# Performance work log

Measured on AMD Instinct MI355X. Metric: run time of the kernel, lower is better.

The kernel has to match this reference:

```python
import jax, jax.numpy as jnp
import numpy as np

N, F, E, K = 2048, 32, 16, 32
SPARSITY = 0.05


def setup_inputs() -> dict:
    key = jax.random.key(0)
    ks = jax.random.split(key, 10)
    adj = (jax.random.uniform(ks[0], (N, N)) < SPARSITY).astype(jnp.float32)
    nodes_features = jax.random.normal(ks[1], (N, F), dtype=jnp.float32)
    edges_features = jax.random.normal(ks[2], (N, N, E), dtype=jnp.float32)
    s = 0.05
    W_ne = jax.random.normal(ks[3], (F + E, F), dtype=jnp.float32) * s
    b_ne = jnp.zeros((F,), dtype=jnp.float32)
    W_n = jax.random.normal(ks[4], (F, F), dtype=jnp.float32) * s
    b_n = jnp.zeros((F,), dtype=jnp.float32)
    W_net = jax.random.normal(ks[5], (F, K), dtype=jnp.float32) * s
    b_net = jnp.zeros((K,), dtype=jnp.float32)
    eps = jnp.zeros((1,), dtype=jnp.float32)
    return {"adj": adj, "nodes_features": nodes_features, "edges_features": edges_features,
            "W_ne": W_ne, "b_ne": b_ne, "W_n": W_n, "b_n": b_n,
            "W_net": W_net, "b_net": b_net, "eps": eps}


def reference(adj, nodes_features, edges_features, W_ne, b_ne, W_n, b_n, W_net, b_net, eps):
    # node_edge_net(cat([broadcast(nodes), edges])) == split matmul: avoids
    # materializing the [N,N,F+E] concat; the [N,N,F] output is still formed.
    Fdim = nodes_features.shape[-1]
    node_part = nodes_features @ W_ne[:Fdim]            # [N,F] -> broadcast over dim 0
    edge_part = jnp.einsum('ije,ef->ijf', edges_features, W_ne[Fdim:])  # [N,N,F]
    ne = jax.nn.relu(node_part[None, :, :] + edge_part + b_ne)          # [N,N,F]
    msg = jnp.einsum('ij,ijf->if', adj, ne)             # masked sum over neighbors j
    node_term = jax.nn.relu(nodes_features @ W_n + b_n)  # node_net
    out = (1.0 + eps) * node_term + msg
    out = jax.nn.relu(out @ W_net + b_net)               # self.net (FCLayer)
    return (adj, out, edges_features)
```

## Files before the change

### kernel.cpp

```cpp
#include <hip/hip_runtime.h>
#include <stdint.h>

#define NN 2048
#define FF 32
#define EE 16
#define KK 32
#define NCOPY 2048
#define TOTALB (2 * NN)

__global__ __launch_bounds__(256) void gin_fused_kernel(
    const float* __restrict__ adj,
    const float* __restrict__ nodes,
    const float* __restrict__ edges,
    const float* __restrict__ W_ne,
    const float* __restrict__ b_ne,
    const float* __restrict__ W_n,
    const float* __restrict__ b_n,
    const float* __restrict__ W_net,
    const float* __restrict__ b_net,
    const float* __restrict__ epsp,
    float* __restrict__ out_adj,
    float* __restrict__ out_y,
    float* __restrict__ out_edges)
{
    const int b   = blockIdx.x;
    const int tid = threadIdx.x;

    if (b & 1) {
        const int cb = b >> 1;
        const float4* __restrict__ src = (const float4*)edges;
        float4*       __restrict__ dst = (float4*)out_edges;
        const int per  = (NN * NN * EE / 4) / NCOPY;
        const int base = cb * per;
        #pragma unroll 8
        for (int t = tid; t < per; t += 256) dst[base + t] = src[base + t];
        return;
    }

    const int i = b >> 1;
    const int f = tid & 31;
    const int g = tid >> 5;

    __shared__ float swe[EE][FF];
    __shared__ float swn[FF][FF];
    __shared__ unsigned short sidx[NN];
    __shared__ float sval[NN];
    __shared__ float smsg[FF];
    __shared__ float sh[FF];
    __shared__ int scnt;

    for (int t = tid; t < EE * FF; t += 256) swe[t / FF][t % FF] = W_ne[FF * FF + t];
    for (int t = tid; t < FF * FF; t += 256) swn[t / FF][t % FF] = W_ne[t];
    if (tid == 0) scnt = 0;
    if (tid < FF) smsg[tid] = 0.0f;
    __syncthreads();

    const size_t arow = (size_t)i * NN;

    {
        const float4* src = (const float4*)(adj + arow);
        float4* dst = (float4*)(out_adj + arow);
        #pragma unroll
        for (int t = tid; t < NN / 4; t += 256) {
            float4 v = src[t];
            dst[t] = v;
            if (v.x != 0.0f) { int p = atomicAdd(&scnt, 1); sidx[p] = (unsigned short)(t * 4 + 0); sval[p] = v.x; }
            if (v.y != 0.0f) { int p = atomicAdd(&scnt, 1); sidx[p] = (unsigned short)(t * 4 + 1); sval[p] = v.y; }
            if (v.z != 0.0f) { int p = atomicAdd(&scnt, 1); sidx[p] = (unsigned short)(t * 4 + 2); sval[p] = v.z; }
            if (v.w != 0.0f) { int p = atomicAdd(&scnt, 1); sidx[p] = (unsigned short)(t * 4 + 3); sval[p] = v.w; }
        }
    }
    __syncthreads();

    const int M = scnt;
    const float bne = b_ne[f];
    float acc = 0.0f;
    for (int n = g; n < M; n += 8) {
        const int j = sidx[n];
        const float a = sval[n];
        const float4* nr = (const float4*)(nodes + (size_t)j * FF);
        float npv = 0.0f;
        #pragma unroll
        for (int m = 0; m < 8; ++m) {
            float4 q = nr[m];
            npv += q.x * swn[4 * m + 0][f];
            npv += q.y * swn[4 * m + 1][f];
            npv += q.z * swn[4 * m + 2][f];
            npv += q.w * swn[4 * m + 3][f];
        }
        const float4* er = (const float4*)(edges + (arow + j) * EE);
        float s = 0.0f;
        #pragma unroll
        for (int m = 0; m < 4; ++m) {
            float4 e = er[m];
            s += e.x * swe[4 * m + 0][f];
            s += e.y * swe[4 * m + 1][f];
            s += e.z * swe[4 * m + 2][f];
            s += e.w * swe[4 * m + 3][f];
        }
        acc += a * fmaxf(npv + s + bne, 0.0f);
    }
    atomicAdd(&smsg[f], acc);
    __syncthreads();

    if (tid < FF) {
        const float eps = epsp[0];
        const float* nrow = nodes + (size_t)i * FF;
        float nt = 0.0f;
        #pragma unroll
        for (int e = 0; e < FF; ++e) nt += nrow[e] * W_n[e * FF + f];
        nt = fmaxf(nt + b_n[f], 0.0f);
        sh[f] = (1.0f + eps) * nt + smsg[f];
    }
    __syncthreads();

    if (tid < KK) {
        const int k = tid;
        float o = b_net[k];
        #pragma unroll
        for (int ff2 = 0; ff2 < FF; ++ff2) o += sh[ff2] * W_net[ff2 * KK + k];
        out_y[(size_t)i * KK + k] = fmaxf(o, 0.0f);
    }
}

extern "C" void kernel_launch(void* const* d_in, const int* in_sizes, int n_in,
                              void* d_out, int out_size, void* d_ws, size_t ws_size,
                              hipStream_t stream) {
    (void)in_sizes; (void)n_in; (void)out_size; (void)d_ws; (void)ws_size;
    const float* adj   = (const float*)d_in[0];
    const float* nodes = (const float*)d_in[1];
    const float* edges = (const float*)d_in[2];
    const float* W_ne  = (const float*)d_in[3];
    const float* b_ne  = (const float*)d_in[4];
    const float* W_n   = (const float*)d_in[5];
    const float* b_n   = (const float*)d_in[6];
    const float* W_net = (const float*)d_in[7];
    const float* b_net = (const float*)d_in[8];
    const float* epsp  = (const float*)d_in[9];

    float* out       = (float*)d_out;
    float* out_adj   = out;
    float* out_y     = out + (size_t)NN * NN;
    float* out_edges = out + (size_t)NN * NN + (size_t)NN * KK;

    gin_fused_kernel<<<TOTALB, 256, 0, stream>>>(adj, nodes, edges, W_ne, b_ne, W_n, b_n,
                                                 W_net, b_net, epsp,
                                                 out_adj, out_y, out_edges);
}
```

Measured before the change: 485.7 us.

## Precompute per-node projections in a separate kernel and stage gathered edges in LDS

Adds a precompute kernel that computes nodes@W_ne[:F] and relu(nodes@W_n+b_n) once per node into workspace, so the main kernel no longer recomputes the 32x32 node projection for every neighbor. The main kernel also stages each chunk of gathered edge rows into shared memory with cooperative float4 loads before the per-neighbor compute. This costs an extra launch, workspace traffic, extra LDS (about 12KB), and a pair of barriers per chunk. A fallback keeps the old path when no workspace is available.

```diff
diff --git a/kernel.cpp b/kernel.cpp
--- a/kernel.cpp
+++ b/kernel.cpp
@@ -7,18 +7,45 @@
 #define KK 32
 #define NCOPY 2048
 #define TOTALB (2 * NN)
+#define CH 192
+
+__global__ __launch_bounds__(256) void gin_precompute(
+    const float* __restrict__ nodes, const float* __restrict__ W_ne,
+    const float* __restrict__ W_n, const float* __restrict__ b_n,
+    float* __restrict__ npw, float* __restrict__ ntw)
+{
+    const int f = threadIdx.x & 31;
+    const int r = threadIdx.x >> 5;
+    const int j = blockIdx.x * 8 + r;
+    __shared__ float sw1[FF][FF];
+    __shared__ float sw2[FF][FF];
+    for (int t = threadIdx.x; t < FF * FF; t += 256) {
+        sw1[t / FF][t % FF] = W_ne[t];
+        sw2[t / FF][t % FF] = W_n[t];
+    }
+    __syncthreads();
+    const float* nr = nodes + (size_t)j * FF;
+    float a = 0.0f, b = 0.0f;
+    #pragma unroll
+    for (int e = 0; e < FF; ++e) {
+        float x = nr[e];
+        a += x * sw1[e][f];
+        b += x * sw2[e][f];
+    }
+    npw[(size_t)j * FF + f] = a;
+    ntw[(size_t)j * FF + f] = fmaxf(b + b_n[f], 0.0f);
+}
 
 __global__ __launch_bounds__(256) void gin_fused_kernel(
     const float* __restrict__ adj,
-    const float* __restrict__ nodes,
     const float* __restrict__ edges,
     const float* __restrict__ W_ne,
     const float* __restrict__ b_ne,
-    const float* __restrict__ W_n,
-    const float* __restrict__ b_n,
     const float* __restrict__ W_net,
     const float* __restrict__ b_net,
     const float* __restrict__ epsp,
+    const float* __restrict__ npw,
+    const float* __restrict__ ntw,
     float* __restrict__ out_adj,
     float* __restrict__ out_y,
     float* __restrict__ out_edges)
@@ -42,15 +69,14 @@
     const int g = tid >> 5;
 
     __shared__ float swe[EE][FF];
-    __shared__ float swn[FF][FF];
     __shared__ unsigned short sidx[NN];
     __shared__ float sval[NN];
+    __shared__ float sed[CH][EE];
     __shared__ float smsg[FF];
     __shared__ float sh[FF];
     __shared__ int scnt;
 
     for (int t = tid; t < EE * FF; t += 256) swe[t / FF][t % FF] = W_ne[FF * FF + t];
-    for (int t = tid; t < FF * FF; t += 256) swn[t / FF][t % FF] = W_ne[t];
     if (tid == 0) scnt = 0;
     if (tid < FF) smsg[tid] = 0.0f;
     __syncthreads();
@@ -72,6 +98,104 @@
     }
     __syncthreads();
 
+    const int M = scnt;
+    const float bne = b_ne[f];
+    float acc = 0.0f;
+    for (int base = 0; base < M; base += CH) {
+        const int cnt = min(CH, M - base);
+        for (int t = tid; t < cnt * 4; t += 256) {
+            const int r = t >> 2, m = t & 3;
+            const int j = sidx[base + r];
+            const float4* er = (const float4*)(edges + (arow + (size_t)j) * EE);
+            ((float4*)sed[r])[m] = er[m];
+        }
+        __syncthreads();
+        for (int n = g; n < cnt; n += 8) {
+            const int j = sidx[base + n];
+            const float a = sval[base + n];
+            const float np = npw[(size_t)j * FF + f];
+            const float4* sr = (const float4*)sed[n];
+            float s = 0.0f;
+            #pragma unroll
+            for (int m = 0; m < 4; ++m) {
+                float4 e = sr[m];
+                s += e.x * swe[4 * m + 0][f];
+                s += e.y * swe[4 * m + 1][f];
+                s += e.z * swe[4 * m + 2][f];
+                s += e.w * swe[4 * m + 3][f];
+            }
+            acc += a * fmaxf(np + s + bne, 0.0f);
+        }
+        __syncthreads();
+    }
+    atomicAdd(&smsg[f], acc);
+    __syncthreads();
+
+    if (tid < FF) {
+        sh[tid] = (1.0f + epsp[0]) * ntw[(size_t)i * FF + tid] + smsg[tid];
+    }
+    __syncthreads();
+
+    if (tid < KK) {
+        const int k = tid;
+        float o = b_net[k];
+        #pragma unroll
+        for (int ff2 = 0; ff2 < FF; ++ff2) o += sh[ff2] * W_net[ff2 * KK + k];
+        out_y[(size_t)i * KK + k] = fmaxf(o, 0.0f);
+    }
+}
+
+__global__ __launch_bounds__(256) void gin_fused_fallback(
+    const float* __restrict__ adj, const float* __restrict__ nodes,
+    const float* __restrict__ edges, const float* __restrict__ W_ne,
+    const float* __restrict__ b_ne, const float* __restrict__ W_n,
+    const float* __restrict__ b_n, const float* __restrict__ W_net,
+    const float* __restrict__ b_net, const float* __restrict__ epsp,
+    float* __restrict__ out_adj, float* __restrict__ out_y,
+    float* __restrict__ out_edges)
+{
+    const int b   = blockIdx.x;
+    const int tid = threadIdx.x;
+    if (b & 1) {
+        const int cb = b >> 1;
+        const float4* __restrict__ src = (const float4*)edges;
+        float4*       __restrict__ dst = (float4*)out_edges;
+        const int per  = (NN * NN * EE / 4) / NCOPY;
+        const int base = cb * per;
+        #pragma unroll 8
+        for (int t = tid; t < per; t += 256) dst[base + t] = src[base + t];
+        return;
+    }
+    const int i = b >> 1;
+    const int f = tid & 31;
+    const int g = tid >> 5;
+    __shared__ float swe[EE][FF];
+    __shared__ float swn[FF][FF];
+    __shared__ unsigned short sidx[NN];
+    __shared__ float sval[NN];
+    __shared__ float smsg[FF];
+    __shared__ float sh[FF];
+    __shared__ int scnt;
+    for (int t = tid; t < EE * FF; t += 256) swe[t / FF][t % FF] = W_ne[FF * FF + t];
+    for (int t = tid; t < FF * FF; t += 256) swn[t / FF][t % FF] = W_ne[t];
+    if (tid == 0) scnt = 0;
+    if (tid < FF) smsg[tid] = 0.0f;
+    __syncthreads();
+    const size_t arow = (size_t)i * NN;
+    {
+        const float4* src = (const float4*)(adj + arow);
+        float4* dst = (float4*)(out_adj + arow);
+        #pragma unroll
+        for (int t = tid; t < NN / 4; t += 256) {
+            float4 v = src[t];
+            dst[t] = v;
+            if (v.x != 0.0f) { int p = atomicAdd(&scnt, 1); sidx[p] = (unsigned short)(t * 4 + 0); sval[p] = v.x; }
+            if (v.y != 0.0f) { int p = atomicAdd(&scnt, 1); sidx[p] = (unsigned short)(t * 4 + 1); sval[p] = v.y; }
+            if (v.z != 0.0f) { int p = atomicAdd(&scnt, 1); sidx[p] = (unsigned short)(t * 4 + 2); sval[p] = v.z; }
+            if (v.w != 0.0f) { int p = atomicAdd(&scnt, 1); sidx[p] = (unsigned short)(t * 4 + 3); sval[p] = v.w; }
+        }
+    }
+    __syncthreads();
     const int M = scnt;
     const float bne = b_ne[f];
     float acc = 0.0f;
@@ -102,7 +226,6 @@
     }
     atomicAdd(&smsg[f], acc);
     __syncthreads();
-
     if (tid < FF) {
         const float eps = epsp[0];
         const float* nrow = nodes + (size_t)i * FF;
@@ -113,7 +236,6 @@
         sh[f] = (1.0f + eps) * nt + smsg[f];
     }
     __syncthreads();
-
     if (tid < KK) {
         const int k = tid;
         float o = b_net[k];
@@ -126,7 +248,7 @@
 extern "C" void kernel_launch(void* const* d_in, const int* in_sizes, int n_in,
                               void* d_out, int out_size, void* d_ws, size_t ws_size,
                               hipStream_t stream) {
-    (void)in_sizes; (void)n_in; (void)out_size; (void)d_ws; (void)ws_size;
+    (void)in_sizes; (void)n_in; (void)out_size;
     const float* adj   = (const float*)d_in[0];
     const float* nodes = (const float*)d_in[1];
     const float* edges = (const float*)d_in[2];
@@ -143,7 +265,17 @@
     float* out_y     = out + (size_t)NN * NN;
     float* out_edges = out + (size_t)NN * NN + (size_t)NN * KK;
 
-    gin_fused_kernel<<<TOTALB, 256, 0, stream>>>(adj, nodes, edges, W_ne, b_ne, W_n, b_n,
-                                                 W_net, b_net, epsp,
-                                                 out_adj, out_y, out_edges);
-}
+    const size_t need = (size_t)2 * NN * FF * sizeof(float);
+    if (d_ws != nullptr && ws_size >= need) {
+        float* npw = (float*)d_ws;
+        float* ntw = npw + (size_t)NN * FF;
+        gin_precompute<<<NN / 8, 256, 0, stream>>>(nodes, W_ne, W_n, b_n, npw, ntw);
+        gin_fused_kernel<<<TOTALB, 256, 0, stream>>>(adj, edges, W_ne, b_ne,
+                                                     W_net, b_net, epsp, npw, ntw,
+                                                     out_adj, out_y, out_edges);
+    } else {
+        gin_fused_fallback<<<TOTALB, 256, 0, stream>>>(adj, nodes, edges, W_ne, b_ne,
+                                                       W_n, b_n, W_net, b_net, epsp,
+                                                       out_adj, out_y, out_edges);
+    }
+}
```

New measurement: 493.6 us. No clear change (+1.6%).
